# Kernel tuning notes

Measured on AMD Instinct MI355X. Metric: run time of the kernel, lower is better.

Reference implementation:

```python
import jax, jax.numpy as jnp
import numpy as np

B, IN, OUT, T = 64, 1024, 512, 512
V_TH = 1.0
TAU = 16.0


def alpha_kernel(t, tau):
    # SRM alpha kernel: (t/tau)*exp(1 - t/tau) for t > 0, else 0.
    # Mask BEFORE exp to avoid overflow for large negative t.
    ts = jnp.where(t > 0, t, tau)
    v = (ts / tau) * jnp.exp(1.0 - ts / tau)
    return jnp.where(t > 0, v, 0.0)


def setup_inputs() -> dict:
    key = jax.random.key(0)
    k1, k2 = jax.random.split(key)
    # input spike times in [0, T/2)
    in_spike = jax.random.uniform(k1, (B, IN), dtype=jnp.float32) * (T / 2)
    weight = jax.random.normal(k2, (OUT, IN), dtype=jnp.float32) / np.float32(np.sqrt(IN))
    return {"in_spike": in_spike, "weight": weight}


def reference(in_spike, weight):
    t_seq = jnp.arange(T, dtype=jnp.float32)                  # [T]
    time_sequence = t_seq[None, None, :] - in_spike[:, :, None]  # [B, in, T]
    v_input = alpha_kernel(time_sequence, TAU)                 # [B, in, T]
    # fc applied along the `in` axis at every time step
    membrane_voltage = jnp.einsum('bit,oi->bot', v_input, weight)  # [B, out, T]
    # first time index where voltage crosses threshold; T if never.
    mask = membrane_voltage >= V_TH                            # [B, out, T]
    spiked = mask.any(axis=-1)
    first_t = jnp.argmax(mask, axis=-1)                        # first True index
    out_spike = jnp.where(spiked, first_t, T).astype(jnp.float32)  # [B, out]
    return out_spike
```

## Files before the change

### kernel.cpp

```cpp
#include <hip/hip_runtime.h>
#include <math.h>

#define BATCH   64
#define INS     1024
#define OUTS    512
#define TSTEPS  512
#define TAUF    16.0f
#define LOG2E_OVER_TAU 0.0901684400555602f

#define TT 64
#define NTRANS ((INS / TT) * (OUTS / TT))

__global__ __launch_bounds__(256) void pre_kernel(
        const float* __restrict__ w, float* __restrict__ wT,
        const float* __restrict__ in_spike, float4* __restrict__ spk,
        int* __restrict__ starts) {
    __shared__ float tile[TT][TT + 1];
    __shared__ int hist[257];
    __shared__ int cursor[257];
    __shared__ int wsum[4];

    if (blockIdx.x < NTRANS) {
        const int i0 = (blockIdx.x & (INS / TT - 1)) * TT;
        const int o0 = (blockIdx.x / (INS / TT)) * TT;
        const int c  = threadIdx.x & 63;
        const int r  = threadIdx.x >> 6;
#pragma unroll
        for (int rr = r; rr < TT; rr += 4)
            tile[rr][c] = w[(o0 + rr) * INS + i0 + c];
        __syncthreads();
#pragma unroll
        for (int rr = r; rr < TT; rr += 4)
            wT[(i0 + rr) * OUTS + o0 + c] = tile[c][rr];
        return;
    }

    const int b = blockIdx.x - NTRANS;
    const int tid = threadIdx.x;
    for (int k = tid; k < 257; k += 256) hist[k] = 0;
    __syncthreads();

    float sv[INS / 256];
    int   tv[INS / 256];
#pragma unroll
    for (int j = 0; j < INS / 256; ++j) {
        int i = tid + j * 256;
        float s = in_spike[b * INS + i];
        sv[j] = s;
        int t = (int)floorf(s) + 1;
        t = t < 1 ? 1 : (t > 256 ? 256 : t);
        tv[j] = t;
        atomicAdd(&hist[t], 1);
    }
    __syncthreads();

    const int lane = tid & 63;
    const int wv   = tid >> 6;
    int v = hist[tid + 1];
    int sc = v;
#pragma unroll
    for (int off = 1; off < 64; off <<= 1) {
        int n = __shfl_up(sc, off, 64);
        if (lane >= off) sc += n;
    }
    if (lane == 63) wsum[wv] = sc;
    __syncthreads();
    int base = 0;
    for (int j = 0; j < wv; ++j) base += wsum[j];
    int excl = sc + base - v;
    cursor[tid + 1] = excl;
    starts[b * 258 + tid + 1] = excl;
    if (tid == 0) { starts[b * 258] = 0; starts[b * 258 + 257] = INS; }
    __syncthreads();

#pragma unroll
    for (int j = 0; j < INS / 256; ++j) {
        int i = tid + j * 256;
        int t = tv[j];
        int pos = atomicAdd(&cursor[t], 1);
        float A = expf(fmaf(sv[j], 1.0f / TAUF, 1.0f)) * (1.0f / TAUF);
        float C = -sv[j] * A;
        spk[b * INS + pos] =
            make_float4(A, __int_as_float(i * (OUTS * 4)), C, __int_as_float(t));
    }
}

#define OL 32
#define G  32
#define WS 8
#define TAIL0 257
#define NGRP 8
#define NG (G / NGRP)

typedef unsigned int u32;

__global__ __launch_bounds__(OL * G, 8) void spike_scan_kernel(
        const float4* __restrict__ spk, const int* __restrict__ starts,
        const float* __restrict__ wT, float* __restrict__ out) {
    const int b = blockIdx.x;
    const int x = threadIdx.x;
    const int g = threadIdx.y;
    const int tid = g * OL + x;

    __shared__ float4 sspk[INS];
    __shared__ float4 sP[G][OL];
    __shared__ float4 sQ[NG][OL];
    __shared__ int    sSt[258];
    __shared__ int    sFirst[2 * OL];

    {
        auto gsrc = (const __attribute__((address_space(1))) u32*)
                        (spk + (size_t)b * INS + tid);
        auto ldst = (__attribute__((address_space(3))) u32*)&sspk[tid];
        __builtin_amdgcn_global_load_lds(gsrc, ldst, 16, 0, 0);
    }
    if (tid < 258) sSt[tid] = starts[b * 258 + tid];
    if (tid < 2 * OL) sFirst[tid] = TSTEPS;
    __syncthreads();

    const int w0 = g * WS + 1;
    const char* __restrict__ wTb =
        (const char*)wT + ((size_t)blockIdx.y * OL) * sizeof(float2);
    const u32 x8 = (u32)(x << 3);

    float cA0 = 0.f, cC0 = 0.f, cA1 = 0.f, cC1 = 0.f;
    float l00, l01, l02, l03, l04, l05, l06, l07;
    float l10, l11, l12, l13, l14, l15, l16, l17;
    int k = sSt[w0];

#define BUCKET(D, LA, LB)                                                     \
    {                                                                         \
        const int e = sSt[w0 + (D) + 1];                                      \
        for (; k + 2 <= e; k += 2) {                                          \
            float4 p0 = sspk[k + 0];                                          \
            float4 p1 = sspk[k + 1];                                          \
            float2 q0 = *(const float2*)(wTb + ((u32)__float_as_int(p0.y) + x8)); \
            float2 q1 = *(const float2*)(wTb + ((u32)__float_as_int(p1.y) + x8)); \
            cA0 = fmaf(q0.x, p0.x, cA0); cC0 = fmaf(q0.x, p0.z, cC0);         \
            cA1 = fmaf(q0.y, p0.x, cA1); cC1 = fmaf(q0.y, p0.z, cC1);         \
            cA0 = fmaf(q1.x, p1.x, cA0); cC0 = fmaf(q1.x, p1.z, cC0);         \
            cA1 = fmaf(q1.y, p1.x, cA1); cC1 = fmaf(q1.y, p1.z, cC1);         \
        }                                                                     \
        if (k < e) {                                                          \
            float4 p = sspk[k];                                               \
            float2 q = *(const float2*)(wTb + ((u32)__float_as_int(p.y) + x8)); \
            cA0 = fmaf(q.x, p.x, cA0); cC0 = fmaf(q.x, p.z, cC0);             \
            cA1 = fmaf(q.y, p.x, cA1); cC1 = fmaf(q.y, p.z, cC1);             \
            ++k;                                                              \
        }                                                                     \
        const float tf = (float)(w0 + (D));                                   \
        LA = fmaf(tf, cA0, cC0);                                              \
        LB = fmaf(tf, cA1, cC1);                                              \
    }

    BUCKET(0, l00, l10)
    BUCKET(1, l01, l11)
    BUCKET(2, l02, l12)
    BUCKET(3, l03, l13)
    BUCKET(4, l04, l14)
    BUCKET(5, l05, l15)
    BUCKET(6, l06, l16)
    BUCKET(7, l07, l17)
#undef BUCKET

    sP[g][x] = make_float4(cA0, cC0, cA1, cC1);
    __syncthreads();

    float SA0 = 0.f, SC0 = 0.f, SA1 = 0.f, SC1 = 0.f;
    {
        const int g0 = g & ~(NGRP - 1);
        for (int j = g0; j < g; ++j) {
            float4 v = sP[j][x];
            SA0 += v.x; SC0 += v.y; SA1 += v.z; SC1 += v.w;
        }
    }
    if ((g & (NGRP - 1)) == (NGRP - 1))
        sQ[g >> 3][x] = make_float4(SA0 + cA0, SC0 + cC0, SA1 + cA1, SC1 + cC1);
    __syncthreads();
    float TA0 = 0.f, TC0 = 0.f, TA1 = 0.f, TC1 = 0.f;
    {
        const int myg = g >> 3;
#pragma unroll
        for (int s = 0; s < NG; ++s) {
            float4 qv = sQ[s][x];
            TA0 += qv.x; TC0 += qv.y; TA1 += qv.z; TC1 += qv.w;
            if (s < myg) {
                SA0 += qv.x; SC0 += qv.y; SA1 += qv.z; SC1 += qv.w;
            }
        }
    }

    unsigned m0 = 0, m1 = 0;
#define CHECK(D, LA, LB)                                                      \
    {                                                                         \
        const float tf = (float)(w0 + (D));                                   \
        const float ev = exp2f(tf * LOG2E_OVER_TAU);                          \
        m0 |= (fmaf(tf, SA0, SC0) + (LA) >= ev) ? (1u << (D)) : 0u;           \
        m1 |= (fmaf(tf, SA1, SC1) + (LB) >= ev) ? (1u << (D)) : 0u;           \
    }
    CHECK(0, l00, l10)
    CHECK(1, l01, l11)
    CHECK(2, l02, l12)
    CHECK(3, l03, l13)
    CHECK(4, l04, l14)
    CHECK(5, l05, l15)
    CHECK(6, l06, l16)
    CHECK(7, l07, l17)
#undef CHECK
    int f0 = m0 ? (w0 + __builtin_ffs(m0) - 1) : TSTEPS;
    int f1 = m1 ? (w0 + __builtin_ffs(m1) - 1) : TSTEPS;

    {
        const int t0 = TAIL0 + g * WS;
        unsigned n0 = 0, n1 = 0;
        float tg = (float)t0;
        for (int d = 0; d < WS; ++d) {
            if (t0 + d < TSTEPS) {
                float ev = exp2f(tg * LOG2E_OVER_TAU);
                n0 |= (fmaf(tg, TA0, TC0) >= ev) ? (1u << d) : 0u;
                n1 |= (fmaf(tg, TA1, TC1) >= ev) ? (1u << d) : 0u;
            }
            tg += 1.0f;
        }
        if (n0) f0 = min(f0, t0 + __builtin_ffs(n0) - 1);
        if (n1) f1 = min(f1, t0 + __builtin_ffs(n1) - 1);
    }

    if (f0 < TSTEPS) atomicMin(&sFirst[2 * x], f0);
    if (f1 < TSTEPS) atomicMin(&sFirst[2 * x + 1], f1);
    __syncthreads();
    if (tid < 2 * OL)
        out[b * OUTS + blockIdx.y * (2 * OL) + tid] = (float)sFirst[tid];
}

extern "C" void kernel_launch(void* const* d_in, const int* in_sizes, int n_in,
                              void* d_out, int out_size, void* d_ws, size_t ws_size,
                              hipStream_t stream) {
    const float* in_spike = (const float*)d_in[0];
    const float* weight   = (const float*)d_in[1];
    float* out = (float*)d_out;

    float*  wT     = (float*)d_ws;
    float4* spk    = (float4*)((char*)d_ws + (size_t)INS * OUTS * sizeof(float));
    int*    starts = (int*)((char*)d_ws + (size_t)INS * OUTS * sizeof(float)
                                        + (size_t)BATCH * INS * sizeof(float4));

    pre_kernel<<<NTRANS + BATCH, 256, 0, stream>>>(weight, wT, in_spike, spk, starts);
    spike_scan_kernel<<<dim3(BATCH, OUTS / (2 * OL)), dim3(OL, G), 0, stream>>>(
        spk, starts, wT, out);
}
```

Baseline: 93.15 us.

## Process four outputs per thread with branchless masked bucket accumulation

The scan kernel now gives each thread four output neurons (float4 weight loads) over a window of four time steps. The per-bucket loop is replaced by one loop over all spikes in the window that uses per-step masks, with zero sentinel spikes padded at the end so it can unroll by four. The goal is more reuse per shared/global load, fewer divergent loop exits and fewer threads per output. In exchange it adds more register pressure, more FMAs per spike from the masking, and changes the grid and block shape.

Measured after the change: 84.11 us. 9.7% less time.

```diff
diff --git a/kernel.cpp b/kernel.cpp
--- a/kernel.cpp
+++ b/kernel.cpp
@@ -85,16 +85,16 @@
     }
 }
 
-#define OL 32
-#define G  32
-#define WS 8
+#define OL 16
+#define G  64
+#define WS 4
 #define TAIL0 257
 #define NGRP 8
 #define NG (G / NGRP)
 
 typedef unsigned int u32;
 
-__global__ __launch_bounds__(OL * G, 8) void spike_scan_kernel(
+__global__ __launch_bounds__(OL * G, 4) void spike_scan_kernel(
         const float4* __restrict__ spk, const int* __restrict__ starts,
         const float* __restrict__ wT, float* __restrict__ out) {
     const int b = blockIdx.x;
@@ -102,11 +102,13 @@
     const int g = threadIdx.y;
     const int tid = g * OL + x;
 
-    __shared__ float4 sspk[INS];
-    __shared__ float4 sP[G][OL];
-    __shared__ float4 sQ[NG][OL];
+    __shared__ float4 sspk[INS + 4];
+    __shared__ float4 sPA[G][OL];
+    __shared__ float4 sPC[G][OL];
+    __shared__ float4 sQA[NG][OL];
+    __shared__ float4 sQC[NG][OL];
     __shared__ int    sSt[258];
-    __shared__ int    sFirst[2 * OL];
+    __shared__ int    sFirst[4 * OL];
 
     {
         auto gsrc = (const __attribute__((address_space(1))) u32*)
@@ -114,123 +116,136 @@
         auto ldst = (__attribute__((address_space(3))) u32*)&sspk[tid];
         __builtin_amdgcn_global_load_lds(gsrc, ldst, 16, 0, 0);
     }
+    if (tid < 4)
+        sspk[INS + tid] = make_float4(0.f, __int_as_float(0),
+                                      0.f, __int_as_float(1 << 30));
     if (tid < 258) sSt[tid] = starts[b * 258 + tid];
-    if (tid < 2 * OL) sFirst[tid] = TSTEPS;
+    if (tid < 4 * OL) sFirst[tid] = TSTEPS;
     __syncthreads();
 
     const int w0 = g * WS + 1;
     const char* __restrict__ wTb =
-        (const char*)wT + ((size_t)blockIdx.y * OL) * sizeof(float2);
-    const u32 x8 = (u32)(x << 3);
-
-    float cA0 = 0.f, cC0 = 0.f, cA1 = 0.f, cC1 = 0.f;
-    float l00, l01, l02, l03, l04, l05, l06, l07;
-    float l10, l11, l12, l13, l14, l15, l16, l17;
-    int k = sSt[w0];
-
-#define BUCKET(D, LA, LB)                                                     \
-    {                                                                         \
-        const int e = sSt[w0 + (D) + 1];                                      \
-        for (; k + 2 <= e; k += 2) {                                          \
-            float4 p0 = sspk[k + 0];                                          \
-            float4 p1 = sspk[k + 1];                                          \
-            float2 q0 = *(const float2*)(wTb + ((u32)__float_as_int(p0.y) + x8)); \
-            float2 q1 = *(const float2*)(wTb + ((u32)__float_as_int(p1.y) + x8)); \
-            cA0 = fmaf(q0.x, p0.x, cA0); cC0 = fmaf(q0.x, p0.z, cC0);         \
-            cA1 = fmaf(q0.y, p0.x, cA1); cC1 = fmaf(q0.y, p0.z, cC1);         \
-            cA0 = fmaf(q1.x, p1.x, cA0); cC0 = fmaf(q1.x, p1.z, cC0);         \
-            cA1 = fmaf(q1.y, p1.x, cA1); cC1 = fmaf(q1.y, p1.z, cC1);         \
-        }                                                                     \
-        if (k < e) {                                                          \
-            float4 p = sspk[k];                                               \
-            float2 q = *(const float2*)(wTb + ((u32)__float_as_int(p.y) + x8)); \
-            cA0 = fmaf(q.x, p.x, cA0); cC0 = fmaf(q.x, p.z, cC0);             \
-            cA1 = fmaf(q.y, p.x, cA1); cC1 = fmaf(q.y, p.z, cC1);             \
-            ++k;                                                              \
-        }                                                                     \
-        const float tf = (float)(w0 + (D));                                   \
-        LA = fmaf(tf, cA0, cC0);                                              \
-        LB = fmaf(tf, cA1, cC1);                                              \
-    }
-
-    BUCKET(0, l00, l10)
-    BUCKET(1, l01, l11)
-    BUCKET(2, l02, l12)
-    BUCKET(3, l03, l13)
-    BUCKET(4, l04, l14)
-    BUCKET(5, l05, l15)
-    BUCKET(6, l06, l16)
-    BUCKET(7, l07, l17)
-#undef BUCKET
-
-    sP[g][x] = make_float4(cA0, cC0, cA1, cC1);
-    __syncthreads();
-
-    float SA0 = 0.f, SC0 = 0.f, SA1 = 0.f, SC1 = 0.f;
+        (const char*)wT + (size_t)blockIdx.y * (4 * OL) * sizeof(float);
+    const u32 x16 = (u32)(x << 4);
+
+    const int s = sSt[w0];
+    const int e = sSt[w0 + WS];
+
+    float4 PA[WS], PC[WS];
+#pragma unroll
+    for (int d = 0; d < WS; ++d) {
+        PA[d] = make_float4(0.f, 0.f, 0.f, 0.f);
+        PC[d] = make_float4(0.f, 0.f, 0.f, 0.f);
+    }
+
+    for (int k = s; k < e; k += 4) {
+#pragma unroll
+        for (int j = 0; j < 4; ++j) {
+            const float4 p = sspk[k + j];
+            const float4 q = *(const float4*)(
+                wTb + ((u32)__float_as_int(p.y) + x16));
+            const int ton = __float_as_int(p.w);
+#pragma unroll
+            for (int d = 0; d < WS; ++d) {
+                const bool on = (ton <= w0 + d);
+                const float Ad = on ? p.x : 0.0f;
+                const float Cd = on ? p.z : 0.0f;
+                PA[d].x = fmaf(q.x, Ad, PA[d].x);
+                PC[d].x = fmaf(q.x, Cd, PC[d].x);
+                PA[d].y = fmaf(q.y, Ad, PA[d].y);
+                PC[d].y = fmaf(q.y, Cd, PC[d].y);
+                PA[d].z = fmaf(q.z, Ad, PA[d].z);
+                PC[d].z = fmaf(q.z, Cd, PC[d].z);
+                PA[d].w = fmaf(q.w, Ad, PA[d].w);
+                PC[d].w = fmaf(q.w, Cd, PC[d].w);
+            }
+        }
+    }
+
+    sPA[g][x] = PA[WS - 1];
+    sPC[g][x] = PC[WS - 1];
+    __syncthreads();
+
+    float4 SA = make_float4(0.f, 0.f, 0.f, 0.f);
+    float4 SC = make_float4(0.f, 0.f, 0.f, 0.f);
     {
         const int g0 = g & ~(NGRP - 1);
         for (int j = g0; j < g; ++j) {
-            float4 v = sP[j][x];
-            SA0 += v.x; SC0 += v.y; SA1 += v.z; SC1 += v.w;
-        }
-    }
-    if ((g & (NGRP - 1)) == (NGRP - 1))
-        sQ[g >> 3][x] = make_float4(SA0 + cA0, SC0 + cC0, SA1 + cA1, SC1 + cC1);
-    __syncthreads();
-    float TA0 = 0.f, TC0 = 0.f, TA1 = 0.f, TC1 = 0.f;
+            float4 a = sPA[j][x], c = sPC[j][x];
+            SA.x += a.x; SA.y += a.y; SA.z += a.z; SA.w += a.w;
+            SC.x += c.x; SC.y += c.y; SC.z += c.z; SC.w += c.w;
+        }
+    }
+    if ((g & (NGRP - 1)) == (NGRP - 1)) {
+        sQA[g >> 3][x] = make_float4(SA.x + PA[WS-1].x, SA.y + PA[WS-1].y,
+                                     SA.z + PA[WS-1].z, SA.w + PA[WS-1].w);
+        sQC[g >> 3][x] = make_float4(SC.x + PC[WS-1].x, SC.y + PC[WS-1].y,
+                                     SC.z + PC[WS-1].z, SC.w + PC[WS-1].w);
+    }
+    __syncthreads();
+    float4 TA = make_float4(0.f, 0.f, 0.f, 0.f);
+    float4 TC = make_float4(0.f, 0.f, 0.f, 0.f);
     {
         const int myg = g >> 3;
 #pragma unroll
-        for (int s = 0; s < NG; ++s) {
-            float4 qv = sQ[s][x];
-            TA0 += qv.x; TC0 += qv.y; TA1 += qv.z; TC1 += qv.w;
-            if (s < myg) {
-                SA0 += qv.x; SC0 += qv.y; SA1 += qv.z; SC1 += qv.w;
+        for (int ss = 0; ss < NG; ++ss) {
+            float4 qa = sQA[ss][x], qc = sQC[ss][x];
+            TA.x += qa.x; TA.y += qa.y; TA.z += qa.z; TA.w += qa.w;
+            TC.x += qc.x; TC.y += qc.y; TC.z += qc.z; TC.w += qc.w;
+            if (ss < myg) {
+                SA.x += qa.x; SA.y += qa.y; SA.z += qa.z; SA.w += qa.w;
+                SC.x += qc.x; SC.y += qc.y; SC.z += qc.z; SC.w += qc.w;
             }
         }
     }
 
-    unsigned m0 = 0, m1 = 0;
-#define CHECK(D, LA, LB)                                                      \
-    {                                                                         \
-        const float tf = (float)(w0 + (D));                                   \
-        const float ev = exp2f(tf * LOG2E_OVER_TAU);                          \
-        m0 |= (fmaf(tf, SA0, SC0) + (LA) >= ev) ? (1u << (D)) : 0u;           \
-        m1 |= (fmaf(tf, SA1, SC1) + (LB) >= ev) ? (1u << (D)) : 0u;           \
-    }
-    CHECK(0, l00, l10)
-    CHECK(1, l01, l11)
-    CHECK(2, l02, l12)
-    CHECK(3, l03, l13)
-    CHECK(4, l04, l14)
-    CHECK(5, l05, l15)
-    CHECK(6, l06, l16)
-    CHECK(7, l07, l17)
-#undef CHECK
+    u32 m0 = 0, m1 = 0, m2 = 0, m3 = 0;
+#pragma unroll
+    for (int d = 0; d < WS; ++d) {
+        const float tf = (float)(w0 + d);
+        const float ev = exp2f(tf * LOG2E_OVER_TAU);
+        m0 |= (fmaf(tf, SA.x, SC.x) + fmaf(tf, PA[d].x, PC[d].x) >= ev)
+                  ? (1u << d) : 0u;
+        m1 |= (fmaf(tf, SA.y, SC.y) + fmaf(tf, PA[d].y, PC[d].y) >= ev)
+                  ? (1u << d) : 0u;
+        m2 |= (fmaf(tf, SA.z, SC.z) + fmaf(tf, PA[d].z, PC[d].z) >= ev)
+                  ? (1u << d) : 0u;
+        m3 |= (fmaf(tf, SA.w, SC.w) + fmaf(tf, PA[d].w, PC[d].w) >= ev)
+                  ? (1u << d) : 0u;
+    }
     int f0 = m0 ? (w0 + __builtin_ffs(m0) - 1) : TSTEPS;
     int f1 = m1 ? (w0 + __builtin_ffs(m1) - 1) : TSTEPS;
+    int f2 = m2 ? (w0 + __builtin_ffs(m2) - 1) : TSTEPS;
+    int f3 = m3 ? (w0 + __builtin_ffs(m3) - 1) : TSTEPS;
 
     {
         const int t0 = TAIL0 + g * WS;
-        unsigned n0 = 0, n1 = 0;
+        u32 n0 = 0, n1 = 0, n2 = 0, n3 = 0;
         float tg = (float)t0;
+#pragma unroll
         for (int d = 0; d < WS; ++d) {
             if (t0 + d < TSTEPS) {
-                float ev = exp2f(tg * LOG2E_OVER_TAU);
-                n0 |= (fmaf(tg, TA0, TC0) >= ev) ? (1u << d) : 0u;
-                n1 |= (fmaf(tg, TA1, TC1) >= ev) ? (1u << d) : 0u;
+                const float ev = exp2f(tg * LOG2E_OVER_TAU);
+                n0 |= (fmaf(tg, TA.x, TC.x) >= ev) ? (1u << d) : 0u;
+                n1 |= (fmaf(tg, TA.y, TC.y) >= ev) ? (1u << d) : 0u;
+                n2 |= (fmaf(tg, TA.z, TC.z) >= ev) ? (1u << d) : 0u;
+                n3 |= (fmaf(tg, TA.w, TC.w) >= ev) ? (1u << d) : 0u;
             }
             tg += 1.0f;
         }
         if (n0) f0 = min(f0, t0 + __builtin_ffs(n0) - 1);
         if (n1) f1 = min(f1, t0 + __builtin_ffs(n1) - 1);
-    }
-
-    if (f0 < TSTEPS) atomicMin(&sFirst[2 * x], f0);
-    if (f1 < TSTEPS) atomicMin(&sFirst[2 * x + 1], f1);
-    __syncthreads();
-    if (tid < 2 * OL)
-        out[b * OUTS + blockIdx.y * (2 * OL) + tid] = (float)sFirst[tid];
+        if (n2) f2 = min(f2, t0 + __builtin_ffs(n2) - 1);
+        if (n3) f3 = min(f3, t0 + __builtin_ffs(n3) - 1);
+    }
+
+    if (f0 < TSTEPS) atomicMin(&sFirst[4 * x + 0], f0);
+    if (f1 < TSTEPS) atomicMin(&sFirst[4 * x + 1], f1);
+    if (f2 < TSTEPS) atomicMin(&sFirst[4 * x + 2], f2);
+    if (f3 < TSTEPS) atomicMin(&sFirst[4 * x + 3], f3);
+    __syncthreads();
+    if (tid < 4 * OL)
+        out[b * OUTS + blockIdx.y * (4 * OL) + tid] = (float)sFirst[tid];
 }
 
 extern "C" void kernel_launch(void* const* d_in, const int* in_sizes, int n_in,
@@ -246,6 +261,6 @@
                                         + (size_t)BATCH * INS * sizeof(float4));
 
     pre_kernel<<<NTRANS + BATCH, 256, 0, stream>>>(weight, wT, in_spike, spk, starts);
-    spike_scan_kernel<<<dim3(BATCH, OUTS / (2 * OL)), dim3(OL, G), 0, stream>>>(
+    spike_scan_kernel<<<dim3(BATCH, OUTS / (4 * OL)), dim3(OL, G), 0, stream>>>(
         spk, starts, wT, out);
 }
```

## Stage weight slice in LDS, shrink output tile, use wave-shuffle prefix scans

Applied to the files above, without the earlier changes.

The scan kernel now copies a 1024x16 slice of the transposed weights into shared memory with global_load_lds, so the gathered weight reads come from LDS instead of scattered global loads. The block shape changes to 8 outputs-pairs by 128 time groups of 2 steps each, and the launch grid grows to 32 output blocks per batch row. Prefix sums over time groups are done with warp shuffles plus a small two-level shared-memory scan instead of serial shared-memory loops, and the spike records are split into compact A/C and row arrays. In exchange, every block reloads 64KB of weights, which adds global traffic and shared-memory pressure that limits occupancy.

Result: faster. 87.61 us (-6.0%).

```diff
diff --git a/kernel.cpp b/kernel.cpp
--- a/kernel.cpp
+++ b/kernel.cpp
@@ -7,6 +7,8 @@
 #define TSTEPS  512
 #define TAUF    16.0f
 #define LOG2E_OVER_TAU 0.0901684400555602f
+
+typedef unsigned int u32;
 
 #define TT 64
 #define NTRANS ((INS / TT) * (OUTS / TT))
@@ -81,18 +83,14 @@
         float A = expf(fmaf(sv[j], 1.0f / TAUF, 1.0f)) * (1.0f / TAUF);
         float C = -sv[j] * A;
         spk[b * INS + pos] =
-            make_float4(A, __int_as_float(i * (OUTS * 4)), C, __int_as_float(t));
+            make_float4(A, __int_as_float(i * 64), C, __int_as_float(t));
     }
 }
 
-#define OL 32
-#define G  32
-#define WS 8
+#define OL 8
+#define G  128
+#define OBLK 16
 #define TAIL0 257
-#define NGRP 8
-#define NG (G / NGRP)
-
-typedef unsigned int u32;
 
 __global__ __launch_bounds__(OL * G, 8) void spike_scan_kernel(
         const float4* __restrict__ spk, const int* __restrict__ starts,
@@ -101,136 +99,162 @@
     const int x = threadIdx.x;
     const int g = threadIdx.y;
     const int tid = g * OL + x;
-
-    __shared__ float4 sspk[INS];
-    __shared__ float4 sP[G][OL];
-    __shared__ float4 sQ[NG][OL];
+    const int lane = tid & 63;
+    const int gl = lane >> 3;
+    const int wv = tid >> 6;
+
+    __shared__ float  ws[INS][OBLK];
+    __shared__ float2 sAC[INS];
+    __shared__ unsigned short sRowB[INS];
+    __shared__ float4 sQ[16][OL];
+    __shared__ float4 sQpre[17][OL];
     __shared__ int    sSt[258];
-    __shared__ int    sFirst[2 * OL];
-
-    {
-        auto gsrc = (const __attribute__((address_space(1))) u32*)
-                        (spk + (size_t)b * INS + tid);
-        auto ldst = (__attribute__((address_space(3))) u32*)&sspk[tid];
-        __builtin_amdgcn_global_load_lds(gsrc, ldst, 16, 0, 0);
+    __shared__ int    sFirst[OBLK];
+
+    {
+        const char* srcb = (const char*)wT
+            + (size_t)(tid >> 2) * (OUTS * 4)
+            + (size_t)blockIdx.y * (OBLK * 4)
+            + (size_t)(tid & 3) * 16;
+        char* dstb = (char*)ws + (size_t)tid * 16;
+#pragma unroll
+        for (int s = 0; s < 4; ++s) {
+            auto gsrc = (const __attribute__((address_space(1))) u32*)
+                            (srcb + (size_t)s * 256 * (OUTS * 4));
+            auto ldst = (__attribute__((address_space(3))) u32*)
+                            (dstb + s * 16384);
+            __builtin_amdgcn_global_load_lds(gsrc, ldst, 16, 0, 0);
+        }
+    }
+    {
+        float4 p = spk[(size_t)b * INS + tid];
+        sAC[tid] = make_float2(p.x, p.z);
+        sRowB[tid] = (unsigned short)__float_as_int(p.y);
     }
     if (tid < 258) sSt[tid] = starts[b * 258 + tid];
-    if (tid < 2 * OL) sFirst[tid] = TSTEPS;
-    __syncthreads();
-
-    const int w0 = g * WS + 1;
-    const char* __restrict__ wTb =
-        (const char*)wT + ((size_t)blockIdx.y * OL) * sizeof(float2);
+    if (tid < OBLK) sFirst[tid] = TSTEPS;
+    __syncthreads();
+
+    const int w0 = 2 * g + 1;
     const u32 x8 = (u32)(x << 3);
-
     float cA0 = 0.f, cC0 = 0.f, cA1 = 0.f, cC1 = 0.f;
-    float l00, l01, l02, l03, l04, l05, l06, l07;
-    float l10, l11, l12, l13, l14, l15, l16, l17;
+    float l00, l01, l10, l11;
     int k = sSt[w0];
-
-#define BUCKET(D, LA, LB)                                                     \
-    {                                                                         \
-        const int e = sSt[w0 + (D) + 1];                                      \
-        for (; k + 2 <= e; k += 2) {                                          \
-            float4 p0 = sspk[k + 0];                                          \
-            float4 p1 = sspk[k + 1];                                          \
-            float2 q0 = *(const float2*)(wTb + ((u32)__float_as_int(p0.y) + x8)); \
-            float2 q1 = *(const float2*)(wTb + ((u32)__float_as_int(p1.y) + x8)); \
-            cA0 = fmaf(q0.x, p0.x, cA0); cC0 = fmaf(q0.x, p0.z, cC0);         \
-            cA1 = fmaf(q0.y, p0.x, cA1); cC1 = fmaf(q0.y, p0.z, cC1);         \
-            cA0 = fmaf(q1.x, p1.x, cA0); cC0 = fmaf(q1.x, p1.z, cC0);         \
-            cA1 = fmaf(q1.y, p1.x, cA1); cC1 = fmaf(q1.y, p1.z, cC1);         \
-        }                                                                     \
-        if (k < e) {                                                          \
-            float4 p = sspk[k];                                               \
-            float2 q = *(const float2*)(wTb + ((u32)__float_as_int(p.y) + x8)); \
-            cA0 = fmaf(q.x, p.x, cA0); cC0 = fmaf(q.x, p.z, cC0);             \
-            cA1 = fmaf(q.y, p.x, cA1); cC1 = fmaf(q.y, p.z, cC1);             \
-            ++k;                                                              \
-        }                                                                     \
-        const float tf = (float)(w0 + (D));                                   \
-        LA = fmaf(tf, cA0, cC0);                                              \
-        LB = fmaf(tf, cA1, cC1);                                              \
-    }
-
-    BUCKET(0, l00, l10)
-    BUCKET(1, l01, l11)
-    BUCKET(2, l02, l12)
-    BUCKET(3, l03, l13)
-    BUCKET(4, l04, l14)
-    BUCKET(5, l05, l15)
-    BUCKET(6, l06, l16)
-    BUCKET(7, l07, l17)
-#undef BUCKET
-
-    sP[g][x] = make_float4(cA0, cC0, cA1, cC1);
-    __syncthreads();
-
-    float SA0 = 0.f, SC0 = 0.f, SA1 = 0.f, SC1 = 0.f;
-    {
-        const int g0 = g & ~(NGRP - 1);
-        for (int j = g0; j < g; ++j) {
-            float4 v = sP[j][x];
-            SA0 += v.x; SC0 += v.y; SA1 += v.z; SC1 += v.w;
-        }
-    }
-    if ((g & (NGRP - 1)) == (NGRP - 1))
-        sQ[g >> 3][x] = make_float4(SA0 + cA0, SC0 + cC0, SA1 + cA1, SC1 + cC1);
-    __syncthreads();
-    float TA0 = 0.f, TC0 = 0.f, TA1 = 0.f, TC1 = 0.f;
-    {
-        const int myg = g >> 3;
-#pragma unroll
-        for (int s = 0; s < NG; ++s) {
-            float4 qv = sQ[s][x];
-            TA0 += qv.x; TC0 += qv.y; TA1 += qv.z; TC1 += qv.w;
-            if (s < myg) {
-                SA0 += qv.x; SC0 += qv.y; SA1 += qv.z; SC1 += qv.w;
+    {
+        const int e0 = sSt[w0 + 1];
+        for (; k < e0; ++k) {
+            float2 ac = sAC[k];
+            u32 ro = (u32)sRowB[k];
+            const float2 q = *(const float2*)((const char*)ws + ro + x8);
+            cA0 = fmaf(q.x, ac.x, cA0); cC0 = fmaf(q.x, ac.y, cC0);
+            cA1 = fmaf(q.y, ac.x, cA1); cC1 = fmaf(q.y, ac.y, cC1);
+        }
+        const float tf = (float)w0;
+        l00 = fmaf(tf, cA0, cC0);
+        l10 = fmaf(tf, cA1, cC1);
+    }
+    {
+        const int e1 = sSt[w0 + 2];
+        for (; k < e1; ++k) {
+            float2 ac = sAC[k];
+            u32 ro = (u32)sRowB[k];
+            const float2 q = *(const float2*)((const char*)ws + ro + x8);
+            cA0 = fmaf(q.x, ac.x, cA0); cC0 = fmaf(q.x, ac.y, cC0);
+            cA1 = fmaf(q.y, ac.x, cA1); cC1 = fmaf(q.y, ac.y, cC1);
+        }
+        const float tf = (float)(w0 + 1);
+        l01 = fmaf(tf, cA0, cC0);
+        l11 = fmaf(tf, cA1, cC1);
+    }
+
+    float sA0 = cA0, sC0 = cC0, sA1 = cA1, sC1 = cC1;
+#pragma unroll
+    for (int off = 8; off <= 32; off <<= 1) {
+        float t0 = __shfl_up(sA0, off);
+        float t1 = __shfl_up(sC0, off);
+        float t2 = __shfl_up(sA1, off);
+        float t3 = __shfl_up(sC1, off);
+        if (lane >= off) { sA0 += t0; sC0 += t1; sA1 += t2; sC1 += t3; }
+    }
+    float eA0 = __shfl_up(sA0, 8);
+    float eC0 = __shfl_up(sC0, 8);
+    float eA1 = __shfl_up(sA1, 8);
+    float eC1 = __shfl_up(sC1, 8);
+    if (gl == 0) { eA0 = 0.f; eC0 = 0.f; eA1 = 0.f; eC1 = 0.f; }
+    if (gl == 7) sQ[wv][x] = make_float4(sA0, sC0, sA1, sC1);
+    __syncthreads();
+
+    if (tid < 64) {
+        const int w = tid >> 3, xx = tid & 7;
+        float4 q1 = sQ[w][xx];
+        float4 q2 = sQ[w + 8][xx];
+        float4 s1 = q1, s2 = q2;
+#pragma unroll
+        for (int off = 8; off <= 32; off <<= 1) {
+            float a0 = __shfl_up(s1.x, off), a1 = __shfl_up(s1.y, off);
+            float a2 = __shfl_up(s1.z, off), a3 = __shfl_up(s1.w, off);
+            float b0 = __shfl_up(s2.x, off), b1 = __shfl_up(s2.y, off);
+            float b2 = __shfl_up(s2.z, off), b3 = __shfl_up(s2.w, off);
+            if (lane >= off) {
+                s1.x += a0; s1.y += a1; s1.z += a2; s1.w += a3;
+                s2.x += b0; s2.y += b1; s2.z += b2; s2.w += b3;
             }
         }
-    }
-
-    unsigned m0 = 0, m1 = 0;
-#define CHECK(D, LA, LB)                                                      \
-    {                                                                         \
-        const float tf = (float)(w0 + (D));                                   \
-        const float ev = exp2f(tf * LOG2E_OVER_TAU);                          \
-        m0 |= (fmaf(tf, SA0, SC0) + (LA) >= ev) ? (1u << (D)) : 0u;           \
-        m1 |= (fmaf(tf, SA1, SC1) + (LB) >= ev) ? (1u << (D)) : 0u;           \
-    }
-    CHECK(0, l00, l10)
-    CHECK(1, l01, l11)
-    CHECK(2, l02, l12)
-    CHECK(3, l03, l13)
-    CHECK(4, l04, l14)
-    CHECK(5, l05, l15)
-    CHECK(6, l06, l16)
-    CHECK(7, l07, l17)
-#undef CHECK
-    int f0 = m0 ? (w0 + __builtin_ffs(m0) - 1) : TSTEPS;
-    int f1 = m1 ? (w0 + __builtin_ffs(m1) - 1) : TSTEPS;
-
-    {
-        const int t0 = TAIL0 + g * WS;
-        unsigned n0 = 0, n1 = 0;
-        float tg = (float)t0;
-        for (int d = 0; d < WS; ++d) {
-            if (t0 + d < TSTEPS) {
-                float ev = exp2f(tg * LOG2E_OVER_TAU);
-                n0 |= (fmaf(tg, TA0, TC0) >= ev) ? (1u << d) : 0u;
-                n1 |= (fmaf(tg, TA1, TC1) >= ev) ? (1u << d) : 0u;
-            }
-            tg += 1.0f;
-        }
-        if (n0) f0 = min(f0, t0 + __builtin_ffs(n0) - 1);
-        if (n1) f1 = min(f1, t0 + __builtin_ffs(n1) - 1);
-    }
-
-    if (f0 < TSTEPS) atomicMin(&sFirst[2 * x], f0);
-    if (f1 < TSTEPS) atomicMin(&sFirst[2 * x + 1], f1);
-    __syncthreads();
-    if (tid < 2 * OL)
-        out[b * OUTS + blockIdx.y * (2 * OL) + tid] = (float)sFirst[tid];
+        float4 h1;
+        h1.x = __shfl(s1.x, 56 + xx); h1.y = __shfl(s1.y, 56 + xx);
+        h1.z = __shfl(s1.z, 56 + xx); h1.w = __shfl(s1.w, 56 + xx);
+        sQpre[w][xx] = make_float4(s1.x - q1.x, s1.y - q1.y,
+                                   s1.z - q1.z, s1.w - q1.w);
+        sQpre[w + 8][xx] = make_float4(h1.x + s2.x - q2.x, h1.y + s2.y - q2.y,
+                                       h1.z + s2.z - q2.z, h1.w + s2.w - q2.w);
+        if (w == 7)
+            sQpre[16][xx] = make_float4(h1.x + s2.x, h1.y + s2.y,
+                                        h1.z + s2.z, h1.w + s2.w);
+    }
+    __syncthreads();
+
+    const float4 pr = sQpre[wv][x];
+    const float4 tt = sQpre[16][x];
+    const float SexA0 = pr.x + eA0, SexC0 = pr.y + eC0;
+    const float SexA1 = pr.z + eA1, SexC1 = pr.w + eC1;
+    int f0 = TSTEPS, f1 = TSTEPS;
+    {
+        const float tf1 = (float)(w0 + 1);
+        const float ev1 = exp2f(tf1 * LOG2E_OVER_TAU);
+        if (fmaf(tf1, SexA0, SexC0) + l01 >= ev1) f0 = w0 + 1;
+        if (fmaf(tf1, SexA1, SexC1) + l11 >= ev1) f1 = w0 + 1;
+        const float tf0 = (float)w0;
+        const float ev0 = exp2f(tf0 * LOG2E_OVER_TAU);
+        if (fmaf(tf0, SexA0, SexC0) + l00 >= ev0) f0 = w0;
+        if (fmaf(tf0, SexA1, SexC1) + l10 >= ev0) f1 = w0;
+    }
+    {
+        const int t0i = TAIL0 + 2 * g;
+        const float ta0 = (float)t0i;
+        const float ta1 = ta0 + 1.0f;
+        const float ev0t = exp2f(ta0 * LOG2E_OVER_TAU);
+        const float ev1t = exp2f(ta1 * LOG2E_OVER_TAU);
+        const bool in1 = (t0i + 1 < TSTEPS);
+        bool c00 = fmaf(ta0, tt.x, tt.y) >= ev0t;
+        bool c01 = in1 && (fmaf(ta1, tt.x, tt.y) >= ev1t);
+        bool c10 = fmaf(ta0, tt.z, tt.w) >= ev0t;
+        bool c11 = in1 && (fmaf(ta1, tt.z, tt.w) >= ev1t);
+        if (f0 == TSTEPS) f0 = c00 ? t0i : (c01 ? t0i + 1 : TSTEPS);
+        if (f1 == TSTEPS) f1 = c10 ? t0i : (c11 ? t0i + 1 : TSTEPS);
+    }
+
+#pragma unroll
+    for (int off = 8; off <= 32; off <<= 1) {
+        f0 = min(f0, __shfl_xor(f0, off));
+        f1 = min(f1, __shfl_xor(f1, off));
+    }
+    if (gl == 0) {
+        if (f0 < TSTEPS) atomicMin(&sFirst[2 * x], f0);
+        if (f1 < TSTEPS) atomicMin(&sFirst[2 * x + 1], f1);
+    }
+    __syncthreads();
+    if (tid < OBLK)
+        out[b * OUTS + blockIdx.y * OBLK + tid] = (float)sFirst[tid];
 }
 
 extern "C" void kernel_launch(void* const* d_in, const int* in_sizes, int n_in,
@@ -246,6 +270,6 @@
                                         + (size_t)BATCH * INS * sizeof(float4));
 
     pre_kernel<<<NTRANS + BATCH, 256, 0, stream>>>(weight, wT, in_spike, spk, starts);
-    spike_scan_kernel<<<dim3(BATCH, OUTS / (2 * OL)), dim3(OL, G), 0, stream>>>(
+    spike_scan_kernel<<<dim3(BATCH, OUTS / OBLK), dim3(OL, G), 0, stream>>>(
         spk, starts, wT, out);
 }
```

## Retile spike scan to 16 outputs x 64 time groups, reduce first-spike via shuffles

Applied to the files above, without the earlier changes.

Each scan block now covers 32 outputs instead of 64 and splits the head window into 64 groups of 4 time steps instead of 32 groups of 8. The grid is swapped so output slices of the same batch run in consecutive blocks. First-spike indices are min-reduced with wave shuffles before fewer LDS atomics, and the transpose tile shrinks to 32x32. The aim is more parallelism, shorter serial bucket chains, better wT locality and less atomic contention. The cost is twice as many blocks, each reloading the batch's spike list into LDS, and a deeper prefix-sum reduction over more groups.

Measured after the change: 89.48 us. 1.04x faster.

```diff
diff --git a/kernel.cpp b/kernel.cpp
--- a/kernel.cpp
+++ b/kernel.cpp
@@ -8,7 +8,9 @@
 #define TAUF    16.0f
 #define LOG2E_OVER_TAU 0.0901684400555602f
 
-#define TT 64
+typedef unsigned int u32;
+
+#define TT 32
 #define NTRANS ((INS / TT) * (OUTS / TT))
 
 __global__ __launch_bounds__(256) void pre_kernel(
@@ -23,14 +25,14 @@
     if (blockIdx.x < NTRANS) {
         const int i0 = (blockIdx.x & (INS / TT - 1)) * TT;
         const int o0 = (blockIdx.x / (INS / TT)) * TT;
-        const int c  = threadIdx.x & 63;
-        const int r  = threadIdx.x >> 6;
-#pragma unroll
-        for (int rr = r; rr < TT; rr += 4)
+        const int c  = threadIdx.x & (TT - 1);
+        const int r  = threadIdx.x >> 5;
+#pragma unroll
+        for (int rr = r; rr < TT; rr += 8)
             tile[rr][c] = w[(o0 + rr) * INS + i0 + c];
         __syncthreads();
 #pragma unroll
-        for (int rr = r; rr < TT; rr += 4)
+        for (int rr = r; rr < TT; rr += 8)
             wT[(i0 + rr) * OUTS + o0 + c] = tile[c][rr];
         return;
     }
@@ -85,22 +87,22 @@
     }
 }
 
-#define OL 32
-#define G  32
-#define WS 8
+#define OL 16
+#define G  64
+#define WS 4
 #define TAIL0 257
 #define NGRP 8
 #define NG (G / NGRP)
 
-typedef unsigned int u32;
-
 __global__ __launch_bounds__(OL * G, 8) void spike_scan_kernel(
         const float4* __restrict__ spk, const int* __restrict__ starts,
         const float* __restrict__ wT, float* __restrict__ out) {
-    const int b = blockIdx.x;
+    const int slice = blockIdx.x;
+    const int b = blockIdx.y;
     const int x = threadIdx.x;
     const int g = threadIdx.y;
     const int tid = g * OL + x;
+    const int lane = tid & 63;
 
     __shared__ float4 sspk[INS];
     __shared__ float4 sP[G][OL];
@@ -119,13 +121,12 @@
     __syncthreads();
 
     const int w0 = g * WS + 1;
-    const char* __restrict__ wTb =
-        (const char*)wT + ((size_t)blockIdx.y * OL) * sizeof(float2);
+    const char* __restrict__ wTb = (const char*)wT + (size_t)slice * (2 * OL) * 4;
     const u32 x8 = (u32)(x << 3);
 
     float cA0 = 0.f, cC0 = 0.f, cA1 = 0.f, cC1 = 0.f;
-    float l00, l01, l02, l03, l04, l05, l06, l07;
-    float l10, l11, l12, l13, l14, l15, l16, l17;
+    float l00, l01, l02, l03;
+    float l10, l11, l12, l13;
     int k = sSt[w0];
 
 #define BUCKET(D, LA, LB)                                                     \
@@ -157,10 +158,6 @@
     BUCKET(1, l01, l11)
     BUCKET(2, l02, l12)
     BUCKET(3, l03, l13)
-    BUCKET(4, l04, l14)
-    BUCKET(5, l05, l15)
-    BUCKET(6, l06, l16)
-    BUCKET(7, l07, l17)
 #undef BUCKET
 
     sP[g][x] = make_float4(cA0, cC0, cA1, cC1);
@@ -202,10 +199,6 @@
     CHECK(1, l01, l11)
     CHECK(2, l02, l12)
     CHECK(3, l03, l13)
-    CHECK(4, l04, l14)
-    CHECK(5, l05, l15)
-    CHECK(6, l06, l16)
-    CHECK(7, l07, l17)
 #undef CHECK
     int f0 = m0 ? (w0 + __builtin_ffs(m0) - 1) : TSTEPS;
     int f1 = m1 ? (w0 + __builtin_ffs(m1) - 1) : TSTEPS;
@@ -214,6 +207,7 @@
         const int t0 = TAIL0 + g * WS;
         unsigned n0 = 0, n1 = 0;
         float tg = (float)t0;
+#pragma unroll
         for (int d = 0; d < WS; ++d) {
             if (t0 + d < TSTEPS) {
                 float ev = exp2f(tg * LOG2E_OVER_TAU);
@@ -226,11 +220,17 @@
         if (n1) f1 = min(f1, t0 + __builtin_ffs(n1) - 1);
     }
 
-    if (f0 < TSTEPS) atomicMin(&sFirst[2 * x], f0);
-    if (f1 < TSTEPS) atomicMin(&sFirst[2 * x + 1], f1);
+    f0 = min(f0, __shfl_xor(f0, 16));
+    f0 = min(f0, __shfl_xor(f0, 32));
+    f1 = min(f1, __shfl_xor(f1, 16));
+    f1 = min(f1, __shfl_xor(f1, 32));
+    if (lane < OL) {
+        if (f0 < TSTEPS) atomicMin(&sFirst[2 * x], f0);
+        if (f1 < TSTEPS) atomicMin(&sFirst[2 * x + 1], f1);
+    }
     __syncthreads();
     if (tid < 2 * OL)
-        out[b * OUTS + blockIdx.y * (2 * OL) + tid] = (float)sFirst[tid];
+        out[b * OUTS + slice * (2 * OL) + tid] = (float)sFirst[tid];
 }
 
 extern "C" void kernel_launch(void* const* d_in, const int* in_sizes, int n_in,
@@ -246,6 +246,6 @@
                                         + (size_t)BATCH * INS * sizeof(float4));
 
     pre_kernel<<<NTRANS + BATCH, 256, 0, stream>>>(weight, wT, in_spike, spk, starts);
-    spike_scan_kernel<<<dim3(BATCH, OUTS / (2 * OL)), dim3(OL, G), 0, stream>>>(
+    spike_scan_kernel<<<dim3(OUTS / (2 * OL), BATCH), dim3(OL, G), 0, stream>>>(
         spk, starts, wT, out);
 }
```
